# Performance work log

Measured on AMD Instinct MI355X. Metric: run time of the kernel, lower is better.

Reference implementation:

```python
import jax, jax.numpy as jnp
import numpy as np

D_MODEL = 768
N_HEADS = 12
D_K = D_MODEL // N_HEADS


def setup_inputs() -> dict:
    key = jax.random.key(0)
    k_x, k_wqkv, k_bqkv, k_wo, k_bo = jax.random.split(key, 5)
    s = 1.0 / np.sqrt(D_MODEL)
    return {
        "x": jax.random.normal(k_x, (2, 4096, D_MODEL), dtype=jnp.float32),
        "w_qkv": jax.random.uniform(k_wqkv, (D_MODEL, 3 * D_MODEL), jnp.float32, -s, s),
        "b_qkv": jax.random.uniform(k_bqkv, (3 * D_MODEL,), jnp.float32, -s, s),
        "w_out": jax.random.uniform(k_wo, (D_MODEL, D_MODEL), jnp.float32, -s, s),
        "b_out": jax.random.uniform(k_bo, (D_MODEL,), jnp.float32, -s, s),
    }


def reference(x, w_qkv, b_qkv, w_out, b_out):
    B, S, E = x.shape
    qkv = x @ w_qkv + b_qkv                                  # [B,S,3E]
    qkv = qkv.reshape(B, S, 3, N_HEADS, D_K)
    qkv = jnp.transpose(qkv, (2, 0, 3, 1, 4))                # [3,B,H,S,Dk]
    q, k, v = qkv[0], qkv[1], qkv[2]
    scores = jnp.einsum("bhsd,bhtd->bhst", q, k) / jnp.sqrt(jnp.float32(D_K))
    attn = jax.nn.softmax(scores, axis=-1)                   # [B,H,S,S]
    ctx = jnp.einsum("bhst,bhtd->bhsd", attn, v)             # [B,H,S,Dk]
    ctx = jnp.transpose(ctx, (0, 2, 1, 3)).reshape(B, S, E)  # [B,S,E]
    return ctx @ w_out + b_out
```

## Files before the change

kernel.cpp:

```cpp
#include <hip/hip_runtime.h>

typedef short short8 __attribute__((ext_vector_type(8)));
typedef float f32x4 __attribute__((ext_vector_type(4)));
typedef float f32x16 __attribute__((ext_vector_type(16)));
typedef unsigned short u16;
typedef unsigned int u32;

__device__ __forceinline__ u16 f2bf(float f) {
  u32 u = __float_as_uint(f);
  u32 r = u + 0x7fffu + ((u >> 16) & 1u);
  return (u16)(r >> 16);
}

__device__ __forceinline__ u32 cvtpk(float lo, float hi) {
  u32 r;
  asm("v_cvt_pk_bf16_f32 %0, %1, %2" : "=v"(r) : "v"(lo), "v"(hi));
  return r;
}

__device__ __forceinline__ void async_copy16(u16* lds_dst, const u16* gsrc) {
  __builtin_amdgcn_global_load_lds(
      (const __attribute__((address_space(1))) u32*)gsrc,
      (__attribute__((address_space(3))) u32*)lds_dst, 16, 0, 0);
}

__global__ void cvt_f32_bf16(const float4* __restrict__ in, uint2* __restrict__ out, int n4) {
  int i = blockIdx.x * blockDim.x + threadIdx.x;
  if (i >= n4) return;
  float4 v = in[i];
  uint2 o;
  o.x = (u32)f2bf(v.x) | ((u32)f2bf(v.y) << 16);
  o.y = (u32)f2bf(v.z) | ((u32)f2bf(v.w) << 16);
  out[i] = o;
}

__global__ __launch_bounds__(256) void cvt_transpose_w(
    const float* __restrict__ W, u16* __restrict__ WT, int K, int N) {
  __shared__ float tl[32 * 33];
  int n0 = blockIdx.x * 32, k0 = blockIdx.y * 32;
  int tx = threadIdx.x & 31, ty = threadIdx.x >> 5;
#pragma unroll
  for (int j = 0; j < 4; ++j)
    tl[(ty + j * 8) * 33 + tx] = W[(size_t)(k0 + ty + j * 8) * N + n0 + tx];
  __syncthreads();
#pragma unroll
  for (int j = 0; j < 4; ++j)
    WT[(size_t)(n0 + ty + j * 8) * K + k0 + tx] = f2bf(tl[tx * 33 + ty + j * 8]);
}

__global__ __launch_bounds__(256) void transpose_v(
    const u16* __restrict__ V, u16* __restrict__ VT) {
  __shared__ u16 tb[64 * 66];
  const int tid = threadIdx.x;
  const int bh = blockIdx.y;
  const int t0 = blockIdx.x * 64;
  const u16* Vb = V + (size_t)bh * 4096 * 64;
  u16* VTb = VT + (size_t)bh * 64 * 4096;
#pragma unroll
  for (int it = 0; it < 2; ++it) {
    int cid = it * 256 + tid;
    int row = cid >> 3, c = cid & 7;
    short8 v = *(const short8*)&Vb[(size_t)(t0 + row) * 64 + c * 8];
#pragma unroll
    for (int i = 0; i < 8; ++i) tb[row * 66 + c * 8 + i] = (u16)v[i];
  }
  __syncthreads();
#pragma unroll
  for (int it = 0; it < 2; ++it) {
    int pid = it * 256 + tid;
    int c2 = pid & 7, d = pid >> 3;
    short8 o;
#pragma unroll
    for (int i = 0; i < 8; ++i) o[i] = (short)tb[(c2 * 8 + i) * 66 + d];
    *(short8*)&VTb[(size_t)d * 4096 + t0 + c2 * 8] = o;
  }
}

#define BM 128
#define BN 128
#define BKG 64

template <int EPI>
__global__ __launch_bounds__(256, 2) void gemm_bf16(
    const u16* __restrict__ A, const u16* __restrict__ Bt,
    const float* __restrict__ bias, int M, int N, int K,
    u16* __restrict__ q_out, u16* __restrict__ k_out, u16* __restrict__ v_out,
    float* __restrict__ c_out) {
  __shared__ u16 lA[BM * BKG];
  __shared__ u16 lB[BN * BKG];
  const int tid = threadIdx.x;
  const int lane = tid & 63;
  const int wid = tid >> 6;
  const int r = lane & 15, hi = lane >> 4;
  const int m0 = blockIdx.y * BM;
  const int n0 = blockIdx.x * BN;
  const int wm = (wid >> 1) * 64;
  const int wn = (wid & 1) * 64;

  f32x4 acc[4][4];
#pragma unroll
  for (int i = 0; i < 4; ++i)
#pragma unroll
    for (int j = 0; j < 4; ++j) acc[i][j] = f32x4{0.f, 0.f, 0.f, 0.f};

  for (int k0 = 0; k0 < K; k0 += BKG) {
#pragma unroll
    for (int j = 0; j < 4; ++j) {
      int cid = j * 256 + tid;
      int row = cid >> 3, c = cid & 7;
      async_copy16(&lA[cid * 8], &A[(size_t)(m0 + row) * K + k0 + c * 8]);
    }
#pragma unroll
    for (int j = 0; j < 4; ++j) {
      int cid = j * 256 + tid;
      int row = cid >> 3, c = cid & 7;
      async_copy16(&lB[cid * 8], &Bt[(size_t)(n0 + row) * K + k0 + c * 8]);
    }
    __syncthreads();
#pragma unroll
    for (int kk = 0; kk < 2; ++kk) {
      short8 af[4], bfr[4];
#pragma unroll
      for (int i = 0; i < 4; ++i)
        af[i] = *(const short8*)&lA[(wm + i * 16 + r) * BKG + kk * 32 + hi * 8];
#pragma unroll
      for (int i = 0; i < 4; ++i)
        bfr[i] = *(const short8*)&lB[(wn + i * 16 + r) * BKG + kk * 32 + hi * 8];
#pragma unroll
      for (int i = 0; i < 4; ++i)
#pragma unroll
        for (int j = 0; j < 4; ++j)
          acc[i][j] = __builtin_amdgcn_mfma_f32_16x16x32_bf16(af[i], bfr[j], acc[i][j], 0, 0, 0);
    }
    __syncthreads();
  }

#pragma unroll
  for (int i = 0; i < 4; ++i) {
#pragma unroll
    for (int j = 0; j < 4; ++j) {
      int gn = n0 + wn + j * 16 + r;
      float bv = bias[gn];
#pragma unroll
      for (int q = 0; q < 4; ++q) {
        int gm = m0 + wm + i * 16 + hi * 4 + q;
        float v = acc[i][j][q] + bv;
        if (EPI == 0) {
          int part = gn / 768;
          int rem = gn - part * 768;
          int h = rem >> 6, d = rem & 63;
          int b = gm >> 12, s = gm & 4095;
          size_t off = (((size_t)(b * 12 + h) * 4096) + s) * 64 + d;
          if (part == 0) q_out[off] = f2bf(v * 0.18033688011112042f);
          else if (part == 1) k_out[off] = f2bf(v);
          else v_out[off] = f2bf(v);
        } else {
          c_out[(size_t)gm * N + gn] = v;
        }
      }
    }
  }
}

__global__ __launch_bounds__(256, 3) void attn_fwd(
    const u16* __restrict__ Qg, const u16* __restrict__ Kg,
    const u16* __restrict__ VTg, u16* __restrict__ ctxg) {
  __shared__ u16 lK[2][64 * 64];
  __shared__ u16 lV[2][64 * 64];
  const int tid = threadIdx.x;
  const int lane = tid & 63, wid = tid >> 6;
  const int q32 = lane & 31, half = lane >> 5;
  const int bh = blockIdx.y;
  const int s0 = blockIdx.x * 128;
  const int qrow = s0 + wid * 32 + q32;
  const u16* Qb = Qg + (size_t)bh * 4096 * 64;
  const u16* Kb = Kg + (size_t)bh * 4096 * 64;
  const u16* Vb = VTg + (size_t)bh * 64 * 4096;

  short8 qf[4];
#pragma unroll
  for (int dc = 0; dc < 4; ++dc)
    qf[dc] = *(const short8*)&Qb[(size_t)qrow * 64 + dc * 16 + half * 8];

  const short8 ones8 = {0x3F80, 0x3F80, 0x3F80, 0x3F80, 0x3F80, 0x3F80, 0x3F80, 0x3F80};
  f32x16 zc;
#pragma unroll
  for (int i = 0; i < 16; ++i) zc[i] = 0.f;

  f32x16 acc0, acc1, acc_l;
#pragma unroll
  for (int i = 0; i < 16; ++i) { acc0[i] = 0.f; acc1[i] = 0.f; acc_l[i] = 0.f; }

#define STAGE(buf, t0_)                                                      \
  do {                                                                       \
    _Pragma("unroll") for (int j = 0; j < 2; ++j) {                          \
      int cid = j * 256 + tid;                                               \
      int row = cid >> 3, c = cid & 7, cs = c ^ (row & 7);                   \
      async_copy16(&lK[buf][cid * 8], &Kb[(size_t)((t0_) + row) * 64 + cs * 8]); \
    }                                                                        \
    _Pragma("unroll") for (int j = 0; j < 2; ++j) {                          \
      int cid = j * 256 + tid;                                               \
      int row = cid >> 3, c = cid & 7, cs = c ^ (row & 7);                   \
      async_copy16(&lV[buf][cid * 8], &Vb[(size_t)row * 4096 + (t0_) + cs * 8]); \
    }                                                                        \
  } while (0)

#define ATTN_TILE(CUR, T0)                                                     \
  {                                                                            \
    __syncthreads();                                                           \
    if ((T0) + 64 < 4096) STAGE((CUR) ^ 1, (T0) + 64);                         \
    const char* lKc = (const char*)lK[CUR];                                    \
    const char* lVc = (const char*)lV[CUR];                                    \
    const int xorq = (q32 & 7);                                                \
    f32x16 sA, sB;                                                             \
    __builtin_amdgcn_s_setprio(1);                                             \
    {                                                                          \
      short8 kA = *(const short8*)(lKc + q32 * 128 + ((half ^ xorq) << 4));    \
      short8 kB = *(const short8*)(lKc + (32 + q32) * 128 + ((half ^ xorq) << 4)); \
      sA = __builtin_amdgcn_mfma_f32_32x32x16_bf16(kA, qf[0], zc, 0, 0, 0);    \
      sB = __builtin_amdgcn_mfma_f32_32x32x16_bf16(kB, qf[0], zc, 0, 0, 0);    \
    }                                                                          \
    _Pragma("unroll") for (int dc = 1; dc < 4; ++dc) {                         \
      int ch = dc * 2 + half;                                                  \
      short8 kA = *(const short8*)(lKc + q32 * 128 + ((ch ^ xorq) << 4));      \
      short8 kB = *(const short8*)(lKc + (32 + q32) * 128 + ((ch ^ xorq) << 4)); \
      sA = __builtin_amdgcn_mfma_f32_32x32x16_bf16(kA, qf[dc], sA, 0, 0, 0);   \
      sB = __builtin_amdgcn_mfma_f32_32x32x16_bf16(kB, qf[dc], sB, 0, 0, 0);   \
    }                                                                          \
    __builtin_amdgcn_s_setprio(0);                                             \
    float pA[16], pB[16];                                                      \
    _Pragma("unroll") for (int i = 0; i < 16; ++i) pA[i] = exp2f(sA[i]);       \
    _Pragma("unroll") for (int i = 0; i < 16; ++i) pB[i] = exp2f(sB[i]);       \
    u32 w0[8], w1[8];                                                          \
    _Pragma("unroll") for (int g = 0; g < 4; ++g) {                            \
      w0[g] = cvtpk(pA[4 * g + 0], pA[4 * g + 1]);                             \
      w1[g] = cvtpk(pA[4 * g + 2], pA[4 * g + 3]);                             \
      w0[4 + g] = cvtpk(pB[4 * g + 0], pB[4 * g + 1]);                         \
      w1[4 + g] = cvtpk(pB[4 * g + 2], pB[4 * g + 3]);                         \
    }                                                                          \
    __builtin_amdgcn_s_setprio(1);                                             \
    _Pragma("unroll") for (int ks = 0; ks < 4; ++ks) {                         \
      u32 x0 = w0[2 * ks], y0 = w0[2 * ks + 1];                                \
      u32 x1 = w1[2 * ks], y1 = w1[2 * ks + 1];                                \
      asm("v_permlane32_swap_b32 %0, %1" : "+v"(x0), "+v"(y0));                \
      asm("v_permlane32_swap_b32 %0, %1" : "+v"(x1), "+v"(y1));                \
      union { u32 u[4]; short8 s; } pa;                                        \
      pa.u[0] = x0; pa.u[1] = x1; pa.u[2] = y0; pa.u[3] = y1;                  \
      {                                                                        \
        int d = q32;                                                           \
        short8 vf = *(const short8*)(lVc + d * 128 + (((ks * 2 + half) ^ (d & 7)) << 4)); \
        acc0 = __builtin_amdgcn_mfma_f32_32x32x16_bf16(pa.s, vf, acc0, 0, 0, 0); \
      }                                                                        \
      {                                                                        \
        int d = 32 + q32;                                                      \
        short8 vf = *(const short8*)(lVc + d * 128 + (((ks * 2 + half) ^ (d & 7)) << 4)); \
        acc1 = __builtin_amdgcn_mfma_f32_32x32x16_bf16(pa.s, vf, acc1, 0, 0, 0); \
      }                                                                        \
      acc_l = __builtin_amdgcn_mfma_f32_32x32x16_bf16(pa.s, ones8, acc_l, 0, 0, 0); \
    }                                                                          \
    __builtin_amdgcn_s_setprio(0);                                             \
  }

  STAGE(0, 0);
  for (int t0 = 0; t0 < 4096; t0 += 128) {
    ATTN_TILE(0, t0);
    ATTN_TILE(1, t0 + 64);
  }

  int b = bh / 12, h = bh - b * 12;
#pragma unroll
  for (int reg = 0; reg < 16; ++reg) {
    int row = (reg & 3) + 8 * (reg >> 2) + 4 * half;
    float iv = 1.f / acc_l[reg];
    size_t base = ((size_t)b * 4096 + s0 + wid * 32 + row) * 768 + h * 64;
    ctxg[base + q32] = f2bf(acc0[reg] * iv);
    ctxg[base + 32 + q32] = f2bf(acc1[reg] * iv);
  }
}

extern "C" void kernel_launch(void* const* d_in, const int* in_sizes, int n_in,
                              void* d_out, int out_size, void* d_ws, size_t ws_size,
                              hipStream_t stream) {
  const float* x = (const float*)d_in[0];
  const float* w_qkv = (const float*)d_in[1];
  const float* b_qkv = (const float*)d_in[2];
  const float* w_out = (const float*)d_in[3];
  const float* b_out = (const float*)d_in[4];
  float* out = (float*)d_out;

  char* ws = (char*)d_ws;
  const size_t SZ_X = (size_t)8192 * 768 * 2;
  const size_t SZ_WQ = (size_t)2304 * 768 * 2;
  const size_t SZ_WO = (size_t)768 * 768 * 2;
  const size_t SZ_HSD = (size_t)24 * 4096 * 64 * 2;
  u16* xb = (u16*)ws;     ws += SZ_X;
  u16* wqkvT = (u16*)ws;  ws += SZ_WQ;
  u16* woutT = (u16*)ws;  ws += SZ_WO;
  u16* Qb = (u16*)ws;     ws += SZ_HSD;
  u16* Kb = (u16*)ws;     ws += SZ_HSD;
  u16* Vb = (u16*)ws;     ws += SZ_HSD;
  u16* VTb = (u16*)ws;    ws += SZ_HSD;
  u16* ctxb = (u16*)ws;   ws += SZ_X;

  cvt_f32_bf16<<<dim3(6144), dim3(256), 0, stream>>>(
      (const float4*)x, (uint2*)xb, 8192 * 768 / 4);
  cvt_transpose_w<<<dim3(72, 24), dim3(256), 0, stream>>>(w_qkv, wqkvT, 768, 2304);
  cvt_transpose_w<<<dim3(24, 24), dim3(256), 0, stream>>>(w_out, woutT, 768, 768);
  gemm_bf16<0><<<dim3(18, 64), dim3(256), 0, stream>>>(
      xb, wqkvT, b_qkv, 8192, 2304, 768, Qb, Kb, Vb, (float*)nullptr);
  transpose_v<<<dim3(64, 24), dim3(256), 0, stream>>>(Vb, VTb);
  attn_fwd<<<dim3(32, 24), dim3(256), 0, stream>>>(Qb, Kb, VTb, ctxb);
  gemm_bf16<1><<<dim3(6, 64), dim3(256), 0, stream>>>(
      ctxb, woutT, b_out, 8192, 768, 768, (u16*)nullptr, (u16*)nullptr, (u16*)nullptr, out);
}
```

Before: 254.1 us.

## Replace ones-MFMA row-sum with scalar fp32 sums and interleave softmax with PV

Drops the extra MFMA against a ones vector that computed the softmax denominator. Each lane now accumulates its exp values in fp32 and combines them across half-waves with a shuffle at the end. The per-tile schedule is also reordered: the sA and sB score chains run one after the other, and exponentiation of each half is interleaved with the PV MFMAs that use it, with the setprio hints removed. This cuts matrix-core work by about a third in the PV phase, at the cost of some VALU adds and a different instruction overlap.

```diff
diff --git a/kernel.cpp b/kernel.cpp
--- a/kernel.cpp
+++ b/kernel.cpp
@@ -176,20 +176,21 @@
   const u16* Qb = Qg + (size_t)bh * 4096 * 64;
   const u16* Kb = Kg + (size_t)bh * 4096 * 64;
   const u16* Vb = VTg + (size_t)bh * 64 * 4096;
+  const int xorq = q32 & 7;
 
   short8 qf[4];
 #pragma unroll
   for (int dc = 0; dc < 4; ++dc)
     qf[dc] = *(const short8*)&Qb[(size_t)qrow * 64 + dc * 16 + half * 8];
 
-  const short8 ones8 = {0x3F80, 0x3F80, 0x3F80, 0x3F80, 0x3F80, 0x3F80, 0x3F80, 0x3F80};
   f32x16 zc;
 #pragma unroll
   for (int i = 0; i < 16; ++i) zc[i] = 0.f;
 
-  f32x16 acc0, acc1, acc_l;
-#pragma unroll
-  for (int i = 0; i < 16; ++i) { acc0[i] = 0.f; acc1[i] = 0.f; acc_l[i] = 0.f; }
+  f32x16 acc0, acc1;
+#pragma unroll
+  for (int i = 0; i < 16; ++i) { acc0[i] = 0.f; acc1[i] = 0.f; }
+  float l_run = 0.f;
 
 #define STAGE(buf, t0_)                                                      \
   do {                                                                       \
@@ -205,60 +206,68 @@
     }                                                                        \
   } while (0)
 
+#define PV_KS(KS)                                                              \
+  {                                                                            \
+    u32 x0 = w0[2 * (KS)], y0 = w0[2 * (KS) + 1];                              \
+    u32 x1 = w1[2 * (KS)], y1 = w1[2 * (KS) + 1];                              \
+    asm("v_permlane32_swap_b32 %0, %1" : "+v"(x0), "+v"(y0));                  \
+    asm("v_permlane32_swap_b32 %0, %1" : "+v"(x1), "+v"(y1));                  \
+    union { u32 u[4]; short8 s; } pa;                                          \
+    pa.u[0] = x0; pa.u[1] = x1; pa.u[2] = y0; pa.u[3] = y1;                    \
+    int ch = (KS) * 2 + half;                                                  \
+    {                                                                          \
+      int d = q32;                                                             \
+      short8 vf = *(const short8*)(lVc + d * 128 + ((ch ^ (d & 7)) << 4));     \
+      acc0 = __builtin_amdgcn_mfma_f32_32x32x16_bf16(pa.s, vf, acc0, 0, 0, 0); \
+    }                                                                          \
+    {                                                                          \
+      int d = 32 + q32;                                                        \
+      short8 vf = *(const short8*)(lVc + d * 128 + ((ch ^ (d & 7)) << 4));     \
+      acc1 = __builtin_amdgcn_mfma_f32_32x32x16_bf16(pa.s, vf, acc1, 0, 0, 0); \
+    }                                                                          \
+  }
+
+#define SM_HALF(S, WOFF)                                                       \
+  _Pragma("unroll") for (int g = 0; g < 4; ++g) {                              \
+    float e0 = exp2f(S[4 * g + 0]), e1 = exp2f(S[4 * g + 1]);                  \
+    float e2 = exp2f(S[4 * g + 2]), e3 = exp2f(S[4 * g + 3]);                  \
+    w0[(WOFF) + g] = cvtpk(e0, e1);                                            \
+    w1[(WOFF) + g] = cvtpk(e2, e3);                                            \
+    ps0 += e0; ps1 += e1; ps2 += e2; ps3 += e3;                                \
+  }
+
 #define ATTN_TILE(CUR, T0)                                                     \
   {                                                                            \
     __syncthreads();                                                           \
     if ((T0) + 64 < 4096) STAGE((CUR) ^ 1, (T0) + 64);                         \
     const char* lKc = (const char*)lK[CUR];                                    \
     const char* lVc = (const char*)lV[CUR];                                    \
-    const int xorq = (q32 & 7);                                                \
     f32x16 sA, sB;                                                             \
-    __builtin_amdgcn_s_setprio(1);                                             \
     {                                                                          \
       short8 kA = *(const short8*)(lKc + q32 * 128 + ((half ^ xorq) << 4));    \
+      sA = __builtin_amdgcn_mfma_f32_32x32x16_bf16(kA, qf[0], zc, 0, 0, 0);    \
+    }                                                                          \
+    _Pragma("unroll") for (int dc = 1; dc < 4; ++dc) {                         \
+      short8 kA = *(const short8*)(lKc + q32 * 128 + (((dc * 2 + half) ^ xorq) << 4)); \
+      sA = __builtin_amdgcn_mfma_f32_32x32x16_bf16(kA, qf[dc], sA, 0, 0, 0);   \
+    }                                                                          \
+    {                                                                          \
       short8 kB = *(const short8*)(lKc + (32 + q32) * 128 + ((half ^ xorq) << 4)); \
-      sA = __builtin_amdgcn_mfma_f32_32x32x16_bf16(kA, qf[0], zc, 0, 0, 0);    \
       sB = __builtin_amdgcn_mfma_f32_32x32x16_bf16(kB, qf[0], zc, 0, 0, 0);    \
     }                                                                          \
     _Pragma("unroll") for (int dc = 1; dc < 4; ++dc) {                         \
-      int ch = dc * 2 + half;                                                  \
-      short8 kA = *(const short8*)(lKc + q32 * 128 + ((ch ^ xorq) << 4));      \
-      short8 kB = *(const short8*)(lKc + (32 + q32) * 128 + ((ch ^ xorq) << 4)); \
-      sA = __builtin_amdgcn_mfma_f32_32x32x16_bf16(kA, qf[dc], sA, 0, 0, 0);   \
+      short8 kB = *(const short8*)(lKc + (32 + q32) * 128 + (((dc * 2 + half) ^ xorq) << 4)); \
       sB = __builtin_amdgcn_mfma_f32_32x32x16_bf16(kB, qf[dc], sB, 0, 0, 0);   \
     }                                                                          \
-    __builtin_amdgcn_s_setprio(0);                                             \
-    float pA[16], pB[16];                                                      \
-    _Pragma("unroll") for (int i = 0; i < 16; ++i) pA[i] = exp2f(sA[i]);       \
-    _Pragma("unroll") for (int i = 0; i < 16; ++i) pB[i] = exp2f(sB[i]);       \
     u32 w0[8], w1[8];                                                          \
-    _Pragma("unroll") for (int g = 0; g < 4; ++g) {                            \
-      w0[g] = cvtpk(pA[4 * g + 0], pA[4 * g + 1]);                             \
-      w1[g] = cvtpk(pA[4 * g + 2], pA[4 * g + 3]);                             \
-      w0[4 + g] = cvtpk(pB[4 * g + 0], pB[4 * g + 1]);                         \
-      w1[4 + g] = cvtpk(pB[4 * g + 2], pB[4 * g + 3]);                         \
-    }                                                                          \
-    __builtin_amdgcn_s_setprio(1);                                             \
-    _Pragma("unroll") for (int ks = 0; ks < 4; ++ks) {                         \
-      u32 x0 = w0[2 * ks], y0 = w0[2 * ks + 1];                                \
-      u32 x1 = w1[2 * ks], y1 = w1[2 * ks + 1];                                \
-      asm("v_permlane32_swap_b32 %0, %1" : "+v"(x0), "+v"(y0));                \
-      asm("v_permlane32_swap_b32 %0, %1" : "+v"(x1), "+v"(y1));                \
-      union { u32 u[4]; short8 s; } pa;                                        \
-      pa.u[0] = x0; pa.u[1] = x1; pa.u[2] = y0; pa.u[3] = y1;                  \
-      {                                                                        \
-        int d = q32;                                                           \
-        short8 vf = *(const short8*)(lVc + d * 128 + (((ks * 2 + half) ^ (d & 7)) << 4)); \
-        acc0 = __builtin_amdgcn_mfma_f32_32x32x16_bf16(pa.s, vf, acc0, 0, 0, 0); \
-      }                                                                        \
-      {                                                                        \
-        int d = 32 + q32;                                                      \
-        short8 vf = *(const short8*)(lVc + d * 128 + (((ks * 2 + half) ^ (d & 7)) << 4)); \
-        acc1 = __builtin_amdgcn_mfma_f32_32x32x16_bf16(pa.s, vf, acc1, 0, 0, 0); \
-      }                                                                        \
-      acc_l = __builtin_amdgcn_mfma_f32_32x32x16_bf16(pa.s, ones8, acc_l, 0, 0, 0); \
-    }                                                                          \
-    __builtin_amdgcn_s_setprio(0);                                             \
+    float ps0 = 0.f, ps1 = 0.f, ps2 = 0.f, ps3 = 0.f;                          \
+    SM_HALF(sA, 0)                                 \
+    PV_KS(0)                                                                   \
+    PV_KS(1)                                                                   \
+    SM_HALF(sB, 4)                              \
+    PV_KS(2)                                                                   \
+    PV_KS(3)                                                                   \
+    l_run += (ps0 + ps1) + (ps2 + ps3);                                        \
   }
 
   STAGE(0, 0);
@@ -267,11 +276,13 @@
     ATTN_TILE(1, t0 + 64);
   }
 
+  float l_tot = l_run + __shfl_xor(l_run, 32);
+  float inv = 1.f / l_tot;
   int b = bh / 12, h = bh - b * 12;
 #pragma unroll
   for (int reg = 0; reg < 16; ++reg) {
     int row = (reg & 3) + 8 * (reg >> 2) + 4 * half;
-    float iv = 1.f / acc_l[reg];
+    float iv = __shfl(inv, row);
     size_t base = ((size_t)b * 4096 + s0 + wid * 32 + row) * 768 + h * 64;
     ctxg[base + q32] = f2bf(acc0[reg] * iv);
     ctxg[base + 32 + q32] = f2bf(acc1[reg] * iv);
```

Result: faster. 244.4 us (-3.8%).
